# Optimization experiments

Hardware: AMD Instinct MI355X
Metric: run time of the kernel (lower is better)

Reference implementation:

```python
import jax, jax.numpy as jnp
import numpy as np

V, D, NH, DH, DFF, NL = 32000, 512, 8, 64, 2048, 6
S, B = 512, 8
NEG = -1e18


def layer_norm(x, g, b, eps=1e-5):
    m = x.mean(-1, keepdims=True)
    v = ((x - m) ** 2).mean(-1, keepdims=True)
    return (x - m) / jnp.sqrt(v + eps) * g + b


def mha(q, k, v, Wq, bq, Wk, bk, Wv, bv, Wo, bo, mask):
    Bq, Q, _ = q.shape
    K = k.shape[1]
    qh = (q @ Wq + bq).reshape(Bq, Q, NH, DH).transpose(0, 2, 1, 3)
    kh = (k @ Wk + bk).reshape(Bq, K, NH, DH).transpose(0, 2, 1, 3)
    vh = (v @ Wv + bv).reshape(Bq, K, NH, DH).transpose(0, 2, 1, 3)
    scores = jnp.einsum('bhqd,bhkd->bhqk', qh, kh) / np.sqrt(DH).astype(np.float32)
    scores = jnp.where(mask[:, None, :, :], NEG, scores)
    attn = jax.nn.softmax(scores, axis=-1)
    ctx = jnp.einsum('bhqk,bhkd->bhqd', attn, vh).transpose(0, 2, 1, 3).reshape(Bq, Q, NH * DH)
    return ctx @ Wo + bo


def positional_encoding(seq_len):
    pos = jnp.arange(seq_len, dtype=jnp.float32)[:, None]
    div = jnp.exp(jnp.arange(0, D, 2, dtype=jnp.float32) * (-np.log(10000.0) / D))
    pe = jnp.zeros((seq_len, D), jnp.float32)
    pe = pe.at[:, 0::2].set(jnp.sin(pos * div))
    pe = pe.at[:, 1::2].set(jnp.cos(pos * div))
    return pe


def setup_inputs() -> dict:
    key = jax.random.key(0)
    ks = iter(jax.random.split(key, 64))
    sc = 0.02
    pn = lambda shape: jax.random.normal(next(ks), shape, jnp.float32) * sc
    inp = {}
    inp['targets'] = jax.random.randint(next(ks), (S, B), 0, V)
    inp['memory'] = jax.random.normal(next(ks), (B, S, D), jnp.float32)
    inp['trg_mask'] = jnp.broadcast_to(jnp.triu(jnp.ones((S, S), bool), 1), (B, S, S))
    inp['memory_mask'] = jnp.zeros((B, S, S), bool)
    emb = pn((V, D)).at[1].set(0.0)  # padding_idx=1
    inp['emb'] = emb
    # stacked per-layer params
    for nm in ['Wq_s', 'Wk_s', 'Wv_s', 'Wo_s', 'Wq_c', 'Wk_c', 'Wv_c', 'Wo_c']:
        inp[nm] = pn((NL, D, D))
    for nm in ['bq_s', 'bk_s', 'bv_s', 'bo_s', 'bq_c', 'bk_c', 'bv_c', 'bo_c']:
        inp[nm] = jnp.zeros((NL, D), jnp.float32)
    inp['W1'] = pn((NL, D, DFF)); inp['b1'] = jnp.zeros((NL, DFF), jnp.float32)
    inp['W2'] = pn((NL, DFF, D)); inp['b2'] = jnp.zeros((NL, D), jnp.float32)
    for nm in ['g1', 'g2', 'g3']:
        inp[nm] = jnp.ones((NL, D), jnp.float32)
    for nm in ['be1', 'be2', 'be3']:
        inp[nm] = jnp.zeros((NL, D), jnp.float32)
    return inp


def reference(targets, memory, trg_mask, memory_mask, emb,
              Wq_s, bq_s, Wk_s, bk_s, Wv_s, bv_s, Wo_s, bo_s,
              Wq_c, bq_c, Wk_c, bk_c, Wv_c, bv_c, Wo_c, bo_c,
              W1, b1, W2, b2, g1, be1, g2, be2, g3, be3):
    # targets: (S, B) ints; embedding + sqrt(d) scale + sinusoidal PE
    x = emb[targets] * np.sqrt(D).astype(np.float32)      # (S, B, D)
    x = x + positional_encoding(targets.shape[0])[:, None, :]
    x = x.transpose(1, 0, 2)                              # (B, S, D)
    for i in range(NL):
        sa = mha(x, x, x, Wq_s[i], bq_s[i], Wk_s[i], bk_s[i], Wv_s[i], bv_s[i],
                 Wo_s[i], bo_s[i], trg_mask)
        x = layer_norm(x + sa, g1[i], be1[i])
        ca = mha(x, memory, memory, Wq_c[i], bq_c[i], Wk_c[i], bk_c[i], Wv_c[i], bv_c[i],
                 Wo_c[i], bo_c[i], memory_mask)
        x = layer_norm(x + ca, g2[i], be2[i])
        ff = jax.nn.relu(x @ W1[i] + b1[i]) @ W2[i] + b2[i]
        x = layer_norm(x + ff, g3[i], be3[i])
    return x
```

## Files before the change

kernel.cpp:

```cpp
#include <hip/hip_runtime.h>

typedef unsigned short u16;
typedef unsigned int   u32;
typedef __attribute__((ext_vector_type(4))) u16   u16x4;
typedef __attribute__((ext_vector_type(8))) u16   u16x8;
typedef __attribute__((ext_vector_type(8))) __bf16 bf16x8;
typedef __attribute__((ext_vector_type(4))) float f32x4;

#define DEV static __device__ __forceinline__

constexpr int DIM = 512, NHEAD = 8, DHEAD = 64, DFFN = 2048, NLAY = 6, SEQ = 512, BATCH = 8;
constexpr int MROWS = BATCH * SEQ;
constexpr long HD = (long)SEQ * DHEAD;
constexpr long SQ = (long)DIM * DIM;

DEV float bf2f(u16 u) { union { u32 i; float f; } x; x.i = (u32)u << 16; return x.f; }
DEV u16 f2bf(float f) { union { float f; u32 i; } x; x.f = f; u32 r = x.i + 0x7fffu + ((x.i >> 16) & 1u); return (u16)(r >> 16); }

DEV void gl_lds16(const u16* g, u16* l) {
    __builtin_amdgcn_global_load_lds((const __attribute__((address_space(1))) u32*)(const void*)g,
                                     (__attribute__((address_space(3))) u32*)(void*)l, 16, 0, 0);
}

struct TP { const float* in[8]; u16* out[8]; long ls[8]; };

__global__ __launch_bounds__(256) void transpose8(TP p)
{
    __shared__ u16 t[32][33];
    int z = blockIdx.z, which = z / NLAY, l = z % NLAY;
    const float* in = p.in[which] + (long)l * SQ;
    u16* out = p.out[which] + (long)l * p.ls[which];
    int k0 = blockIdx.y * 32, n0 = blockIdx.x * 32;
    int tx = threadIdx.x & 31, ty = threadIdx.x >> 5;
    #pragma unroll
    for (int i = ty; i < 32; i += 8) t[i][tx] = f2bf(in[(long)(k0 + i) * 512 + n0 + tx]);
    __syncthreads();
    #pragma unroll
    for (int i = ty; i < 32; i += 8) out[(long)(n0 + i) * 512 + k0 + tx] = t[tx][i];
}

__global__ __launch_bounds__(256) void transpose_w(const float* __restrict__ in, u16* __restrict__ out,
                                                   int K, int N, long outLS)
{
    __shared__ u16 t[32][33];
    long bi = (long)blockIdx.z * K * N, bo = (long)blockIdx.z * outLS;
    int k0 = blockIdx.y * 32, n0 = blockIdx.x * 32;
    int tx = threadIdx.x & 31, ty = threadIdx.x >> 5;
    #pragma unroll
    for (int i = ty; i < 32; i += 8) t[i][tx] = f2bf(in[bi + (long)(k0 + i) * N + n0 + tx]);
    __syncthreads();
    #pragma unroll
    for (int i = ty; i < 32; i += 8) out[bo + (long)(n0 + i) * K + k0 + tx] = t[tx][i];
}

__global__ __launch_bounds__(256) void concat_bias(const float* __restrict__ a, const float* __restrict__ b,
                                                   const float* __restrict__ c, float* __restrict__ out, int nsrc)
{
    int i = blockIdx.x * 256 + threadIdx.x;
    int col = i & 511, j = (i >> 9) % nsrc, l = i / (nsrc * 512);
    const float* s = (j == 0) ? a : (j == 1) ? b : c;
    out[i] = s[l * 512 + col];
}

__global__ __launch_bounds__(256) void conv_f32_bf16(const float* __restrict__ in, u16* __restrict__ out)
{
    long i = ((long)blockIdx.x * 256 + threadIdx.x) * 4;
    float4 v = *(const float4*)(in + i);
    u16x4 o; o.x = f2bf(v.x); o.y = f2bf(v.y); o.z = f2bf(v.z); o.w = f2bf(v.w);
    *(u16x4*)(out + i) = o;
}

__global__ __launch_bounds__(256) void embed_pe(const int* __restrict__ targets, const float* __restrict__ emb,
                                                u16* __restrict__ xb)
{
    int t4 = (blockIdx.x * 256 + threadIdx.x) * 4;
    int d = t4 & (DIM - 1);
    int s = (t4 >> 9) & (SEQ - 1);
    int b = t4 >> 18;
    int tok = targets[s * BATCH + b];
    float4 e = *(const float4*)(emb + (long)tok * DIM + d);
    u16x4 ob;
    const float ef[4] = { e.x, e.y, e.z, e.w };
    #pragma unroll
    for (int j = 0; j < 4; ++j) {
        int dd = d + j;
        float div = expf((float)(dd & ~1) * -0.017988946039016f);
        float ang = (float)s * div;
        float pe = (dd & 1) ? cosf(ang) : sinf(ang);
        ob[j] = f2bf(ef[j] * 22.627416997969522f + pe);
    }
    *(u16x4*)(xb + ((long)b * SEQ + s) * DIM + d) = ob;
}

DEV void scat_sd(u16* dst, int mm, int col, float v) {
    dst[(long)((mm >> 9) * NHEAD + (col >> 6)) * HD + (long)(mm & 511) * DHEAD + (col & 63)] = f2bf(v);
}
DEV void scat_ds(u16* dst, int mm, int col, float v) {
    dst[(long)((mm >> 9) * NHEAD + (col >> 6)) * HD + (long)(col & 63) * SEQ + (mm & 511)] = f2bf(v);
}

template <int BM, int BN, int EPI>
__global__ __launch_bounds__(256) void gemm_t(const u16* __restrict__ A0, const u16* __restrict__ A1,
                                              const u16* __restrict__ Bt,
                                              void* __restrict__ C0, void* __restrict__ C1, void* __restrict__ C2,
                                              const float* __restrict__ bias, int K, int ldc, int gx, int aSplit)
{
    constexpr int NCHA = BM / 8;
    constexpr int NCH  = (BM + BN) / 8;
    constexpr int MI   = BM / 32;
    constexpr int NI   = BN / 32;
    __shared__ __align__(16) u16 lds[2][NCH * 512];

    const int tid = threadIdx.x, lane = tid & 63, wid = tid >> 6;
    const int nwg = gridDim.x, bid = blockIdx.x;
    const int wg = (bid & 7) * (nwg >> 3) + (bid >> 3);
    const int m0 = (wg / gx) * BM, n0 = (wg % gx) * BN;
    const u16* A = (n0 < aSplit) ? A0 : A1;
    const int wr = (wid >> 1) * (BM / 2), wc = (wid & 1) * (BN / 2);
    const int fr = lane & 15, fq = lane >> 4;
    const int srow = lane >> 3;
    const int scol = ((lane & 7) ^ srow) * 8;

    f32x4 acc[MI][NI] = {};

    auto stage = [&](int buf, int k0) {
        #pragma unroll
        for (int c = wid; c < NCH; c += 4) {
            if (c < NCHA) gl_lds16(A  + (long)(m0 + c * 8 + srow) * K + k0 + scol, &lds[buf][c * 512]);
            else          gl_lds16(Bt + (long)(n0 + (c - NCHA) * 8 + srow) * K + k0 + scol, &lds[buf][c * 512]);
        }
    };

    const int nt = K >> 6;
    stage(0, 0);
    __syncthreads();
    int cur = 0;
    const int swz = (fr & 7) << 4;
    for (int t = 0; t < nt; ++t) {
        if (t + 1 < nt) stage(cur ^ 1, (t + 1) << 6);
        const char* lb = (const char*)&lds[cur][0];
        bf16x8 a[MI][2], b[NI][2];
        #pragma unroll
        for (int mi = 0; mi < MI; ++mi)
            #pragma unroll
            for (int kk = 0; kk < 2; ++kk)
                a[mi][kk] = *(const bf16x8*)(lb + (wr + mi * 16 + fr) * 128 + ((kk * 64 + fq * 16) ^ swz));
        #pragma unroll
        for (int ni = 0; ni < NI; ++ni)
            #pragma unroll
            for (int kk = 0; kk < 2; ++kk)
                b[ni][kk] = *(const bf16x8*)(lb + (BM + wc + ni * 16 + fr) * 128 + ((kk * 64 + fq * 16) ^ swz));
        #pragma unroll
        for (int kk = 0; kk < 2; ++kk)
            #pragma unroll
            for (int mi = 0; mi < MI; ++mi)
                #pragma unroll
                for (int ni = 0; ni < NI; ++ni)
                    acc[mi][ni] = __builtin_amdgcn_mfma_f32_16x16x32_bf16(a[mi][kk], b[ni][kk], acc[mi][ni], 0, 0, 0);
        __syncthreads();
        cur ^= 1;
    }

    #pragma unroll
    for (int mi = 0; mi < MI; ++mi)
    #pragma unroll
    for (int ni = 0; ni < NI; ++ni)
    #pragma unroll
    for (int rr = 0; rr < 4; ++rr) {
        int mm = m0 + wr + mi * 16 + fq * 4 + rr;
        int nn = n0 + wc + ni * 16 + fr;
        float v = acc[mi][ni][rr] + bias[nn];
        if (EPI == 0) {
            ((u16*)C0)[(long)mm * ldc + nn] = f2bf(v);
        } else if (EPI == 1) {
            ((u16*)C0)[(long)mm * ldc + nn] = f2bf(fmaxf(v, 0.f));
        } else {
            int which = nn >> 9, col = nn & 511;
            if (which == 0)      scat_sd((u16*)C0, mm, col, v);
            else if (which == 1) scat_sd((u16*)C1, mm, col, v);
            else                 scat_ds((u16*)C2, mm, col, v);
        }
    }
}

template <bool CAUSAL>
__global__ __launch_bounds__(256) void flash_attn(const u16* __restrict__ qh, const u16* __restrict__ kh,
                                                  const u16* __restrict__ vT, u16* __restrict__ ctx)
{
    constexpr int KVB = 128;
    __shared__ __align__(16) u16 Kl[2][KVB * 64];
    __shared__ __align__(16) u16 Vl[2][64 * KVB];
    __shared__ __align__(16) u16 Pl[4][16 * KVB];
    const int lane = threadIdx.x & 63, wid = threadIdx.x >> 6;
    const int head = blockIdx.x & 63, qt = blockIdx.x >> 6;
    const int q0 = qt * 64;
    const long hb = (long)head * HD;
    const int fr = lane & 15, fq = lane >> 4;
    const int swz = (fr & 7) << 4;

    bf16x8 qf[2];
    #pragma unroll
    for (int kf = 0; kf < 2; ++kf)
        qf[kf] = *(const bf16x8*)(qh + hb + (long)(q0 + wid * 16 + fr) * 64 + kf * 32 + fq * 8);

    const int nt = CAUSAL ? (q0 >> 7) + 1 : SEQ / KVB;

    auto stage = [&](int buf, int t) {
        const long kv0 = (long)t * KVB;
        const int kr = lane >> 3;
        const int kcol = ((lane & 7) ^ kr) * 8;
        for (int c = wid; c < 16; c += 4)
            gl_lds16(kh + hb + (kv0 + c * 8 + kr) * 64 + kcol, &Kl[buf][c * 512]);
        const int vr = lane >> 4;
        for (int c = wid; c < 16; c += 4) {
            int row = c * 4 + vr;
            int vcol = ((lane & 15) ^ (row & 7)) * 8;
            gl_lds16(vT + hb + (long)row * SEQ + kv0 + vcol, &Vl[buf][c * 512]);
        }
    };

    float m[4], l[4];
    #pragma unroll
    for (int r = 0; r < 4; ++r) { m[r] = -3.0e38f; l[r] = 0.f; }
    f32x4 ao[4] = {};

    stage(0, 0);
    __syncthreads();
    int cur = 0;
    for (int t = 0; t < nt; ++t) {
        if (t + 1 < nt) stage(cur ^ 1, t + 1);
        f32x4 as[8] = {};
        const char* kb = (const char*)&Kl[cur][0];
        __builtin_amdgcn_s_setprio(1);
        #pragma unroll
        for (int nf = 0; nf < 8; ++nf)
            #pragma unroll
            for (int kf = 0; kf < 2; ++kf) {
                bf16x8 kfr = *(const bf16x8*)(kb + (nf * 16 + fr) * 128 + ((kf * 64 + fq * 16) ^ swz));
                as[nf] = __builtin_amdgcn_mfma_f32_16x16x32_bf16(qf[kf], kfr, as[nf], 0, 0, 0);
            }
        __builtin_amdgcn_s_setprio(0);
        const int kv0 = t * KVB;
        const int qrow = q0 + wid * 16 + fq * 4;
        #pragma unroll
        for (int nf = 0; nf < 8; ++nf)
            #pragma unroll
            for (int rr = 0; rr < 4; ++rr) {
                float s = as[nf][rr] * 0.125f;
                if (CAUSAL && (kv0 + nf * 16 + fr > qrow + rr)) s = -3.0e38f;
                as[nf][rr] = s;
            }
        float p_scale[4];
        #pragma unroll
        for (int rr = 0; rr < 4; ++rr) {
            float mx = as[0][rr];
            #pragma unroll
            for (int nf = 1; nf < 8; ++nf) mx = fmaxf(mx, as[nf][rr]);
            #pragma unroll
            for (int o = 1; o < 16; o <<= 1) mx = fmaxf(mx, __shfl_xor(mx, o, 64));
            float mnew = fmaxf(m[rr], mx);
            p_scale[rr] = __expf(m[rr] - mnew);
            m[rr] = mnew;
        }
        float rsum[4] = {0.f, 0.f, 0.f, 0.f};
        u16* pw = &Pl[wid][0];
        #pragma unroll
        for (int nf = 0; nf < 8; ++nf)
            #pragma unroll
            for (int rr = 0; rr < 4; ++rr) {
                float p = __expf(as[nf][rr] - m[rr]);
                rsum[rr] += p;
                int row = fq * 4 + rr;
                int byte = (row * 256 + (nf * 16 + fr) * 2) ^ ((row & 7) << 4);
                *(u16*)((char*)pw + byte) = f2bf(p);
            }
        #pragma unroll
        for (int rr = 0; rr < 4; ++rr) {
            #pragma unroll
            for (int o = 1; o < 16; o <<= 1) rsum[rr] += __shfl_xor(rsum[rr], o, 64);
            l[rr] = l[rr] * p_scale[rr] + rsum[rr];
        }
        #pragma unroll
        for (int nf = 0; nf < 4; ++nf)
            #pragma unroll
            for (int rr = 0; rr < 4; ++rr) ao[nf][rr] *= p_scale[rr];
        const char* vb = (const char*)&Vl[cur][0];
        __builtin_amdgcn_s_setprio(1);
        #pragma unroll
        for (int kf = 0; kf < 4; ++kf) {
            int pbyte = (fr * 256 + kf * 64 + fq * 16) ^ swz;
            bf16x8 pa = *(const bf16x8*)((const char*)pw + pbyte);
            #pragma unroll
            for (int nf = 0; nf < 4; ++nf) {
                bf16x8 vf = *(const bf16x8*)(vb + (nf * 16 + fr) * 256 + ((kf * 64 + fq * 16) ^ swz));
                ao[nf] = __builtin_amdgcn_mfma_f32_16x16x32_bf16(pa, vf, ao[nf], 0, 0, 0);
            }
        }
        __builtin_amdgcn_s_setprio(0);
        __syncthreads();
        cur ^= 1;
    }
    const int b = head >> 3, h = head & 7;
    #pragma unroll
    for (int nf = 0; nf < 4; ++nf)
        #pragma unroll
        for (int rr = 0; rr < 4; ++rr) {
            int qq = q0 + wid * 16 + fq * 4 + rr;
            ctx[((long)(b * SEQ + qq)) * DIM + h * 64 + nf * 16 + fr] = f2bf(ao[nf][rr] / l[rr]);
        }
}

__global__ __launch_bounds__(256) void add_ln(u16* xb, const u16* __restrict__ y,
                                              const float* __restrict__ g, const float* __restrict__ be,
                                              float* __restrict__ xf)
{
    int row = blockIdx.x * 4 + (threadIdx.x >> 6);
    int lane = threadIdx.x & 63;
    long off = (long)row * DIM + lane * 8;
    u16x8 xv = *(const u16x8*)(xb + off);
    u16x8 yv = *(const u16x8*)(y + off);
    float v[8];
    #pragma unroll
    for (int j = 0; j < 8; ++j) v[j] = bf2f(xv[j]) + bf2f(yv[j]);
    float sum = 0.f;
    #pragma unroll
    for (int j = 0; j < 8; ++j) sum += v[j];
    #pragma unroll
    for (int o = 32; o; o >>= 1) sum += __shfl_xor(sum, o, 64);
    float mean = sum * (1.0f / DIM);
    float vs = 0.f;
    #pragma unroll
    for (int j = 0; j < 8; ++j) { float d = v[j] - mean; vs += d * d; }
    #pragma unroll
    for (int o = 32; o; o >>= 1) vs += __shfl_xor(vs, o, 64);
    float rstd = rsqrtf(vs * (1.0f / DIM) + 1e-5f);
    float outv[8]; u16x8 ob;
    #pragma unroll
    for (int j = 0; j < 8; ++j) {
        int col = lane * 8 + j;
        float r = (v[j] - mean) * rstd * g[col] + be[col];
        outv[j] = r; ob[j] = f2bf(r);
    }
    *(u16x8*)(xb + off) = ob;
    if (xf) {
        *(float4*)(xf + off)     = *(const float4*)&outv[0];
        *(float4*)(xf + off + 4) = *(const float4*)&outv[4];
    }
}

extern "C" void kernel_launch(void* const* d_in, const int* in_sizes, int n_in,
                              void* d_out, int out_size, void* d_ws, size_t ws_size,
                              hipStream_t stream)
{
    const int*   targets = (const int*)  d_in[0];
    const float* memory  = (const float*)d_in[1];
    const float* emb     = (const float*)d_in[4];
    const float* Wg[8]; for (int i = 0; i < 8; ++i) Wg[i] = (const float*)d_in[5 + i];
    const float* bg[8]; for (int i = 0; i < 8; ++i) bg[i] = (const float*)d_in[13 + i];
    const float* W1  = (const float*)d_in[21];
    const float* b1  = (const float*)d_in[22];
    const float* W2  = (const float*)d_in[23];
    const float* b2  = (const float*)d_in[24];
    const float* g1  = (const float*)d_in[25];
    const float* g2  = (const float*)d_in[26];
    const float* g3  = (const float*)d_in[27];
    const float* be1 = (const float*)d_in[28];
    const float* be2 = (const float*)d_in[29];
    const float* be3 = (const float*)d_in[30];

    char* w = (char*)d_ws;
    auto take = [&](size_t n) -> char* { char* p = w; w += (n + 255) & ~(size_t)255; return p; };
    u16*   wqkvT = (u16*)take((size_t)NLAY * 3 * SQ * 2);
    u16*   wcatT = (u16*)take((size_t)NLAY * 3 * SQ * 2);
    u16*   woT   = (u16*)take((size_t)NLAY * SQ * 2);
    u16*   wocT  = (u16*)take((size_t)NLAY * SQ * 2);
    u16*   w1T   = (u16*)take((size_t)NLAY * DIM * DFFN * 2);
    u16*   w2T   = (u16*)take((size_t)NLAY * DIM * DFFN * 2);
    float* bqkv  = (float*)take((size_t)NLAY * 3 * DIM * 4);
    float* bqkvc = (float*)take((size_t)NLAY * 3 * DIM * 4);
    u16*   xb    = (u16*)  take((size_t)MROWS * DIM * 2);
    u16*   y     = (u16*)  take((size_t)MROWS * DIM * 2);
    u16*   memb  = (u16*)  take((size_t)MROWS * DIM * 2);
    u16*   qh    = (u16*)  take((size_t)MROWS * DIM * 2);
    u16*   kh    = (u16*)  take((size_t)MROWS * DIM * 2);
    u16*   vT    = (u16*)  take((size_t)MROWS * DIM * 2);
    u16*   ctx   = (u16*)  take((size_t)MROWS * DIM * 2);
    u16*   h1    = (u16*)  take((size_t)MROWS * DFFN * 2);

    TP tp;
    tp.in[0] = Wg[0]; tp.out[0] = wqkvT;          tp.ls[0] = 3 * SQ;
    tp.in[1] = Wg[1]; tp.out[1] = wqkvT + SQ;     tp.ls[1] = 3 * SQ;
    tp.in[2] = Wg[2]; tp.out[2] = wqkvT + 2 * SQ; tp.ls[2] = 3 * SQ;
    tp.in[3] = Wg[3]; tp.out[3] = woT;            tp.ls[3] = SQ;
    tp.in[4] = Wg[4]; tp.out[4] = wcatT;          tp.ls[4] = 3 * SQ;
    tp.in[5] = Wg[5]; tp.out[5] = wcatT + SQ;     tp.ls[5] = 3 * SQ;
    tp.in[6] = Wg[6]; tp.out[6] = wcatT + 2 * SQ; tp.ls[6] = 3 * SQ;
    tp.in[7] = Wg[7]; tp.out[7] = wocT;           tp.ls[7] = SQ;
    transpose8<<<dim3(16, 16, 8 * NLAY), 256, 0, stream>>>(tp);
    transpose_w<<<dim3(64, 16, NLAY), 256, 0, stream>>>(W1, w1T, DIM, DFFN, (long)DIM * DFFN);
    transpose_w<<<dim3(16, 64, NLAY), 256, 0, stream>>>(W2, w2T, DFFN, DIM, (long)DIM * DFFN);
    concat_bias<<<NLAY * 3 * DIM / 256, 256, 0, stream>>>(bg[0], bg[1], bg[2], bqkv, 3);
    concat_bias<<<NLAY * 3 * DIM / 256, 256, 0, stream>>>(bg[4], bg[5], bg[6], bqkvc, 3);
    conv_f32_bf16<<<2048, 256, 0, stream>>>(memory, memb);
    embed_pe<<<2048, 256, 0, stream>>>(targets, emb, xb);

    const int BIG = 1 << 30;
    for (int i = 0; i < NLAY; ++i) {
        const u16 *wqkv = wqkvT + (long)i * 3 * SQ, *wcat = wcatT + (long)i * 3 * SQ;
        const u16 *wo = woT + (long)i * SQ, *woc = wocT + (long)i * SQ;
        const u16 *w1t = w1T + (long)i * DIM * DFFN, *w2t = w2T + (long)i * DIM * DFFN;
        const float *bo = bg[3] + i * DIM, *boc = bg[7] + i * DIM;

        gemm_t<128, 128, 4><<<384, 256, 0, stream>>>(xb, xb, wqkv, qh, kh, vT, bqkv + i * 3 * DIM, DIM, 0, 12, BIG);
        flash_attn<true><<<BATCH * NHEAD * (SEQ / 64), 256, 0, stream>>>(qh, kh, vT, ctx);
        gemm_t<64, 64, 0><<<512, 256, 0, stream>>>(ctx, ctx, wo, y, nullptr, nullptr, bo, DIM, DIM, 8, BIG);
        add_ln<<<MROWS / 4, 256, 0, stream>>>(xb, y, g1 + i * DIM, be1 + i * DIM, nullptr);

        gemm_t<128, 128, 4><<<384, 256, 0, stream>>>(xb, memb, wcat, qh, kh, vT, bqkvc + i * 3 * DIM, DIM, 0, 12, 512);
        flash_attn<false><<<BATCH * NHEAD * (SEQ / 64), 256, 0, stream>>>(qh, kh, vT, ctx);
        gemm_t<64, 64, 0><<<512, 256, 0, stream>>>(ctx, ctx, woc, y, nullptr, nullptr, boc, DIM, DIM, 8, BIG);
        add_ln<<<MROWS / 4, 256, 0, stream>>>(xb, y, g2 + i * DIM, be2 + i * DIM, nullptr);

        gemm_t<128, 128, 1><<<512, 256, 0, stream>>>(xb, xb, w1t, h1, nullptr, nullptr, b1 + i * DFFN, DIM, DFFN, 16, BIG);
        gemm_t<64, 64, 0><<<512, 256, 0, stream>>>(h1, h1, w2t, y, nullptr, nullptr, b2 + i * DIM, DFFN, DIM, 8, BIG);
        add_ln<<<MROWS / 4, 256, 0, stream>>>(xb, y, g3 + i * DIM, be3 + i * DIM,
                                              (i == NLAY - 1) ? (float*)d_out : nullptr);
    }
}
```

Baseline: 826.0 us.

## Use four-stage LDS ring with K-tile 32 and explicit vmcnt waits in GEMM

The bf16 GEMM moves from a two-buffer, K=64 staging scheme to a four-buffer ring of K=32 tiles. Up to three tiles are kept in flight using global_load_lds. The full __syncthreads after each tile is replaced by an s_waitcnt vmcnt on the outstanding loads plus an s_barrier. The LDS swizzle is reworked for the 64-byte row stride. The aim is to hide global-memory latency behind MFMA work; the cost is more barriers per unit of K, and only a few vmcnt values are supported, so some tile shapes may not compile.

```diff
diff --git a/kernel.cpp b/kernel.cpp
--- a/kernel.cpp
+++ b/kernel.cpp
@@ -20,6 +20,15 @@
 DEV void gl_lds16(const u16* g, u16* l) {
     __builtin_amdgcn_global_load_lds((const __attribute__((address_space(1))) u32*)(const void*)g,
                                      (__attribute__((address_space(3))) u32*)(void*)l, 16, 0, 0);
+}
+
+template <int N> DEV void waitcnt_vm() {
+    if constexpr (N == 0)      asm volatile("s_waitcnt vmcnt(0)" ::: "memory");
+    else if constexpr (N == 2) asm volatile("s_waitcnt vmcnt(2)" ::: "memory");
+    else if constexpr (N == 4) asm volatile("s_waitcnt vmcnt(4)" ::: "memory");
+    else if constexpr (N == 8) asm volatile("s_waitcnt vmcnt(8)" ::: "memory");
+    else static_assert(N == 0, "unsupported vmcnt");
+    __builtin_amdgcn_sched_barrier(0);
 }
 
 struct TP { const float* in[8]; u16* out[8]; long ls[8]; };
@@ -105,11 +114,12 @@
                                               void* __restrict__ C0, void* __restrict__ C1, void* __restrict__ C2,
                                               const float* __restrict__ bias, int K, int ldc, int gx, int aSplit)
 {
-    constexpr int NCHA = BM / 8;
-    constexpr int NCH  = (BM + BN) / 8;
+    constexpr int NCHA = BM / 16;
+    constexpr int NCH  = (BM + BN) / 16;
+    constexpr int CPW  = NCH / 4;
     constexpr int MI   = BM / 32;
     constexpr int NI   = BN / 32;
-    __shared__ __align__(16) u16 lds[2][NCH * 512];
+    __shared__ __align__(16) u16 lds[4][NCH * 512];
 
     const int tid = threadIdx.x, lane = tid & 63, wid = tid >> 6;
     const int nwg = gridDim.x, bid = blockIdx.x;
@@ -118,47 +128,51 @@
     const u16* A = (n0 < aSplit) ? A0 : A1;
     const int wr = (wid >> 1) * (BM / 2), wc = (wid & 1) * (BN / 2);
     const int fr = lane & 15, fq = lane >> 4;
-    const int srow = lane >> 3;
-    const int scol = ((lane & 7) ^ srow) * 8;
+    const int srow = lane >> 2;
+    const int scol = ((lane & 3) ^ ((lane >> 3) & 3)) * 8;
 
     f32x4 acc[MI][NI] = {};
 
     auto stage = [&](int buf, int k0) {
         #pragma unroll
         for (int c = wid; c < NCH; c += 4) {
-            if (c < NCHA) gl_lds16(A  + (long)(m0 + c * 8 + srow) * K + k0 + scol, &lds[buf][c * 512]);
-            else          gl_lds16(Bt + (long)(n0 + (c - NCHA) * 8 + srow) * K + k0 + scol, &lds[buf][c * 512]);
+            if (c < NCHA) gl_lds16(A  + (long)(m0 + c * 16 + srow) * K + k0 + scol, &lds[buf][c * 512]);
+            else          gl_lds16(Bt + (long)(n0 + (c - NCHA) * 16 + srow) * K + k0 + scol, &lds[buf][c * 512]);
         }
     };
 
-    const int nt = K >> 6;
-    stage(0, 0);
-    __syncthreads();
-    int cur = 0;
-    const int swz = (fr & 7) << 4;
+    const int nt = K >> 5;
+    stage(0, 0); stage(1, 32); stage(2, 64);
+    waitcnt_vm<2 * CPW>();
+    __builtin_amdgcn_s_barrier();
+    __builtin_amdgcn_sched_barrier(0);
+
     for (int t = 0; t < nt; ++t) {
-        if (t + 1 < nt) stage(cur ^ 1, (t + 1) << 6);
-        const char* lb = (const char*)&lds[cur][0];
-        bf16x8 a[MI][2], b[NI][2];
+        if (t + 3 < nt) stage((t + 3) & 3, (t + 3) << 5);
+        const char* lb = (const char*)&lds[t & 3][0];
+        bf16x8 a[MI], b[NI];
+        #pragma unroll
+        for (int mi = 0; mi < MI; ++mi) {
+            int row = wr + mi * 16 + fr;
+            a[mi] = *(const bf16x8*)(lb + row * 64 + ((fq * 16) ^ (((row >> 1) & 3) << 4)));
+        }
+        #pragma unroll
+        for (int ni = 0; ni < NI; ++ni) {
+            int row = BM + wc + ni * 16 + fr;
+            b[ni] = *(const bf16x8*)(lb + row * 64 + ((fq * 16) ^ (((row >> 1) & 3) << 4)));
+        }
         #pragma unroll
         for (int mi = 0; mi < MI; ++mi)
             #pragma unroll
-            for (int kk = 0; kk < 2; ++kk)
-                a[mi][kk] = *(const bf16x8*)(lb + (wr + mi * 16 + fr) * 128 + ((kk * 64 + fq * 16) ^ swz));
-        #pragma unroll
-        for (int ni = 0; ni < NI; ++ni)
-            #pragma unroll
-            for (int kk = 0; kk < 2; ++kk)
-                b[ni][kk] = *(const bf16x8*)(lb + (BM + wc + ni * 16 + fr) * 128 + ((kk * 64 + fq * 16) ^ swz));
-        #pragma unroll
-        for (int kk = 0; kk < 2; ++kk)
-            #pragma unroll
-            for (int mi = 0; mi < MI; ++mi)
-                #pragma unroll
-                for (int ni = 0; ni < NI; ++ni)
-                    acc[mi][ni] = __builtin_amdgcn_mfma_f32_16x16x32_bf16(a[mi][kk], b[ni][kk], acc[mi][ni], 0, 0, 0);
-        __syncthreads();
-        cur ^= 1;
+            for (int ni = 0; ni < NI; ++ni)
+                acc[mi][ni] = __builtin_amdgcn_mfma_f32_16x16x32_bf16(a[mi], b[ni], acc[mi][ni], 0, 0, 0);
+        if (t + 1 < nt) {
+            if (t + 3 < nt)       waitcnt_vm<2 * CPW>();
+            else if (t + 3 == nt) waitcnt_vm<CPW>();
+            else                  waitcnt_vm<0>();
+            __builtin_amdgcn_s_barrier();
+            __builtin_amdgcn_sched_barrier(0);
+        }
     }
 
     #pragma unroll
```

Measured after the change: 832.2 us. No clear change (+0.8%).

## Split-K the FFN down-projection GEMM and fuse the reduction into layer norm

Applied to the files above, without the earlier changes.

The W2 GEMM (K=2048) now runs as a two-way split-K over a 2D grid. Each half writes fp32 partial sums without bias into a new buffer. A new add_ln2 kernel sums the two partials, adds the bias and the residual, and applies layer norm. This doubles the workgroup count for the long-K GEMM to improve occupancy and shorten the serial K loop, at the cost of extra fp32 partial traffic (2x4 bytes per element versus 2 bytes for bf16).

```diff
diff --git a/kernel.cpp b/kernel.cpp
--- a/kernel.cpp
+++ b/kernel.cpp
@@ -103,7 +103,8 @@
 __global__ __launch_bounds__(256) void gemm_t(const u16* __restrict__ A0, const u16* __restrict__ A1,
                                               const u16* __restrict__ Bt,
                                               void* __restrict__ C0, void* __restrict__ C1, void* __restrict__ C2,
-                                              const float* __restrict__ bias, int K, int ldc, int gx, int aSplit)
+                                              const float* __restrict__ bias, int K, int ld, int ldc,
+                                              int gx, int aSplit)
 {
     constexpr int NCHA = BM / 8;
     constexpr int NCH  = (BM + BN) / 8;
@@ -116,6 +117,7 @@
     const int wg = (bid & 7) * (nwg >> 3) + (bid >> 3);
     const int m0 = (wg / gx) * BM, n0 = (wg % gx) * BN;
     const u16* A = (n0 < aSplit) ? A0 : A1;
+    const int kBase = blockIdx.y * K;
     const int wr = (wid >> 1) * (BM / 2), wc = (wid & 1) * (BN / 2);
     const int fr = lane & 15, fq = lane >> 4;
     const int srow = lane >> 3;
@@ -126,8 +128,8 @@
     auto stage = [&](int buf, int k0) {
         #pragma unroll
         for (int c = wid; c < NCH; c += 4) {
-            if (c < NCHA) gl_lds16(A  + (long)(m0 + c * 8 + srow) * K + k0 + scol, &lds[buf][c * 512]);
-            else          gl_lds16(Bt + (long)(n0 + (c - NCHA) * 8 + srow) * K + k0 + scol, &lds[buf][c * 512]);
+            if (c < NCHA) gl_lds16(A  + (long)(m0 + c * 8 + srow) * ld + kBase + k0 + scol, &lds[buf][c * 512]);
+            else          gl_lds16(Bt + (long)(n0 + (c - NCHA) * 8 + srow) * ld + kBase + k0 + scol, &lds[buf][c * 512]);
         }
     };
 
@@ -169,11 +171,14 @@
     for (int rr = 0; rr < 4; ++rr) {
         int mm = m0 + wr + mi * 16 + fq * 4 + rr;
         int nn = n0 + wc + ni * 16 + fr;
-        float v = acc[mi][ni][rr] + bias[nn];
+        float v = acc[mi][ni][rr];
+        if (EPI != 5) v += bias[nn];
         if (EPI == 0) {
             ((u16*)C0)[(long)mm * ldc + nn] = f2bf(v);
         } else if (EPI == 1) {
             ((u16*)C0)[(long)mm * ldc + nn] = f2bf(fmaxf(v, 0.f));
+        } else if (EPI == 5) {
+            ((float*)C0)[(long)blockIdx.y * MROWS * ldc + (long)mm * ldc + nn] = v;
         } else {
             int which = nn >> 9, col = nn & 511;
             if (which == 0)      scat_sd((u16*)C0, mm, col, v);
@@ -311,8 +316,7 @@
 }
 
 __global__ __launch_bounds__(256) void add_ln(u16* xb, const u16* __restrict__ y,
-                                              const float* __restrict__ g, const float* __restrict__ be,
-                                              float* __restrict__ xf)
+                                              const float* __restrict__ g, const float* __restrict__ be)
 {
     int row = blockIdx.x * 4 + (threadIdx.x >> 6);
     int lane = threadIdx.x & 63;
@@ -322,6 +326,44 @@
     float v[8];
     #pragma unroll
     for (int j = 0; j < 8; ++j) v[j] = bf2f(xv[j]) + bf2f(yv[j]);
+    float sum = 0.f;
+    #pragma unroll
+    for (int j = 0; j < 8; ++j) sum += v[j];
+    #pragma unroll
+    for (int o = 32; o; o >>= 1) sum += __shfl_xor(sum, o, 64);
+    float mean = sum * (1.0f / DIM);
+    float vs = 0.f;
+    #pragma unroll
+    for (int j = 0; j < 8; ++j) { float d = v[j] - mean; vs += d * d; }
+    #pragma unroll
+    for (int o = 32; o; o >>= 1) vs += __shfl_xor(vs, o, 64);
+    float rstd = rsqrtf(vs * (1.0f / DIM) + 1e-5f);
+    u16x8 ob;
+    #pragma unroll
+    for (int j = 0; j < 8; ++j) {
+        int col = lane * 8 + j;
+        ob[j] = f2bf((v[j] - mean) * rstd * g[col] + be[col]);
+    }
+    *(u16x8*)(xb + off) = ob;
+}
+
+__global__ __launch_bounds__(256) void add_ln2(u16* xb, const float* __restrict__ yf,
+                                               const float* __restrict__ bias,
+                                               const float* __restrict__ g, const float* __restrict__ be,
+                                               float* __restrict__ xf)
+{
+    int row = blockIdx.x * 4 + (threadIdx.x >> 6);
+    int lane = threadIdx.x & 63;
+    long off = (long)row * DIM + lane * 8;
+    u16x8 xv = *(const u16x8*)(xb + off);
+    float4 a0 = *(const float4*)(yf + off);
+    float4 a1 = *(const float4*)(yf + off + 4);
+    float4 b0 = *(const float4*)(yf + (long)MROWS * DIM + off);
+    float4 b1 = *(const float4*)(yf + (long)MROWS * DIM + off + 4);
+    float v[8] = { a0.x + b0.x, a0.y + b0.y, a0.z + b0.z, a0.w + b0.w,
+                   a1.x + b1.x, a1.y + b1.y, a1.z + b1.z, a1.w + b1.w };
+    #pragma unroll
+    for (int j = 0; j < 8; ++j) v[j] += bf2f(xv[j]) + bias[lane * 8 + j];
     float sum = 0.f;
     #pragma unroll
     for (int j = 0; j < 8; ++j) sum += v[j];
@@ -380,6 +422,7 @@
     float* bqkvc = (float*)take((size_t)NLAY * 3 * DIM * 4);
     u16*   xb    = (u16*)  take((size_t)MROWS * DIM * 2);
     u16*   y     = (u16*)  take((size_t)MROWS * DIM * 2);
+    float* yf    = (float*)take((size_t)2 * MROWS * DIM * 4);
     u16*   memb  = (u16*)  take((size_t)MROWS * DIM * 2);
     u16*   qh    = (u16*)  take((size_t)MROWS * DIM * 2);
     u16*   kh    = (u16*)  take((size_t)MROWS * DIM * 2);
@@ -411,19 +454,20 @@
         const u16 *w1t = w1T + (long)i * DIM * DFFN, *w2t = w2T + (long)i * DIM * DFFN;
         const float *bo = bg[3] + i * DIM, *boc = bg[7] + i * DIM;
 
-        gemm_t<128, 128, 4><<<384, 256, 0, stream>>>(xb, xb, wqkv, qh, kh, vT, bqkv + i * 3 * DIM, DIM, 0, 12, BIG);
+        gemm_t<128, 128, 4><<<384, 256, 0, stream>>>(xb, xb, wqkv, qh, kh, vT, bqkv + i * 3 * DIM, DIM, DIM, 0, 12, BIG);
         flash_attn<true><<<BATCH * NHEAD * (SEQ / 64), 256, 0, stream>>>(qh, kh, vT, ctx);
-        gemm_t<64, 64, 0><<<512, 256, 0, stream>>>(ctx, ctx, wo, y, nullptr, nullptr, bo, DIM, DIM, 8, BIG);
-        add_ln<<<MROWS / 4, 256, 0, stream>>>(xb, y, g1 + i * DIM, be1 + i * DIM, nullptr);
-
-        gemm_t<128, 128, 4><<<384, 256, 0, stream>>>(xb, memb, wcat, qh, kh, vT, bqkvc + i * 3 * DIM, DIM, 0, 12, 512);
+        gemm_t<64, 64, 0><<<512, 256, 0, stream>>>(ctx, ctx, wo, y, nullptr, nullptr, bo, DIM, DIM, DIM, 8, BIG);
+        add_ln<<<MROWS / 4, 256, 0, stream>>>(xb, y, g1 + i * DIM, be1 + i * DIM);
+
+        gemm_t<128, 128, 4><<<384, 256, 0, stream>>>(xb, memb, wcat, qh, kh, vT, bqkvc + i * 3 * DIM, DIM, DIM, 0, 12, 512);
         flash_attn<false><<<BATCH * NHEAD * (SEQ / 64), 256, 0, stream>>>(qh, kh, vT, ctx);
-        gemm_t<64, 64, 0><<<512, 256, 0, stream>>>(ctx, ctx, woc, y, nullptr, nullptr, boc, DIM, DIM, 8, BIG);
-        add_ln<<<MROWS / 4, 256, 0, stream>>>(xb, y, g2 + i * DIM, be2 + i * DIM, nullptr);
-
-        gemm_t<128, 128, 1><<<512, 256, 0, stream>>>(xb, xb, w1t, h1, nullptr, nullptr, b1 + i * DFFN, DIM, DFFN, 16, BIG);
-        gemm_t<64, 64, 0><<<512, 256, 0, stream>>>(h1, h1, w2t, y, nullptr, nullptr, b2 + i * DIM, DFFN, DIM, 8, BIG);
-        add_ln<<<MROWS / 4, 256, 0, stream>>>(xb, y, g3 + i * DIM, be3 + i * DIM,
-                                              (i == NLAY - 1) ? (float*)d_out : nullptr);
-    }
-}
+        gemm_t<64, 64, 0><<<512, 256, 0, stream>>>(ctx, ctx, woc, y, nullptr, nullptr, boc, DIM, DIM, DIM, 8, BIG);
+        add_ln<<<MROWS / 4, 256, 0, stream>>>(xb, y, g2 + i * DIM, be2 + i * DIM);
+
+        gemm_t<128, 128, 1><<<512, 256, 0, stream>>>(xb, xb, w1t, h1, nullptr, nullptr, b1 + i * DFFN, DIM, DIM, DFFN, 16, BIG);
+        gemm_t<64, 64, 5><<<dim3(512, 2), 256, 0, stream>>>(h1, h1, w2t, yf, nullptr, nullptr, nullptr,
+                                                            DFFN / 2, DFFN, DIM, 8, BIG);
+        add_ln2<<<MROWS / 4, 256, 0, stream>>>(xb, yf, b2 + i * DIM, g3 + i * DIM, be3 + i * DIM,
+                                               (i == NLAY - 1) ? (float*)d_out : nullptr);
+    }
+}
```

Measured after the change: 817.9 us. Within noise of the previous version (-1.0%).
